# Kernel optimization log

Hardware: AMD Instinct MI355X
Metric: run time of the kernel (lower is better)

## Reference

```python
import jax, jax.numpy as jnp
import numpy as np

TOP_K = 2
NUM_EXPERTS = 64
AUX_COEF = 0.01


def setup_inputs() -> dict:
    key = jax.random.key(0)
    kx, kw = jax.random.split(key)
    B, S, D, E = 4, 4096, 2048, NUM_EXPERTS
    x = jax.random.normal(kx, (B, S, D), dtype=jnp.float32)
    # nn.Linear default init ~ U(-1/sqrt(D), 1/sqrt(D))
    W = jax.random.uniform(kw, (E, D), dtype=jnp.float32,
                           minval=-1.0 / np.sqrt(D), maxval=1.0 / np.sqrt(D))
    return {"x": x, "W": W}


def reference(x, W):
    B, S, D = x.shape
    E = W.shape[0]
    # router projection (no bias)
    logits = jnp.einsum('bsd,ed->bse', x, W)          # [B,S,E]
    probs = jax.nn.softmax(logits, axis=-1)           # [B,S,E]
    top_k_gates, top_k_indices = jax.lax.top_k(probs, TOP_K)  # [B,S,K]
    top_k_gates = top_k_gates / (jnp.sum(top_k_gates, axis=-1, keepdims=True) + 1e-9)
    # aux loss: fraction of routed slots per expert (one-hot mean) x mean router prob
    total_slots = B * S * TOP_K
    counts = jnp.zeros((E,), dtype=jnp.float32).at[top_k_indices.reshape(-1)].add(1.0)
    avg_tokens_per_expert = counts / total_slots      # == one_hot(idx).mean(dims 0,1,2)
    avg_router_prob = jnp.mean(probs, axis=(0, 1))    # [E]
    aux_loss = AUX_COEF * E * jnp.sum(avg_tokens_per_expert * avg_router_prob)
    return top_k_indices, top_k_gates, aux_loss
```

## Files before the change

### kernel.cpp

```cpp
#include <hip/hip_runtime.h>
#include <math.h>

#define NTOK 16384
#define DDIM 2048
#define NEXP 64
#define TM   16
#define NBLK (NTOK / TM)
#define NCH  32
#define NS   64

typedef _Float16 half4v __attribute__((ext_vector_type(4)));
typedef _Float16 half8v __attribute__((ext_vector_type(8)));
typedef float    f32x4  __attribute__((ext_vector_type(4)));

#define MFMA16(a, b, c) __builtin_amdgcn_mfma_f32_16x16x32_f16((a), (b), (c), 0, 0, 0)

__global__ __launch_bounds__(256) void prep_kernel(const float* __restrict__ W,
                                                   _Float16* __restrict__ Wh,
                                                   _Float16* __restrict__ Wl,
                                                   float* __restrict__ accg) {
    int idx = blockIdx.x * 256 + threadIdx.x;
    int e  = idx >> 8;
    int k0 = (idx & 255) << 3;
    const float* wp = W + (size_t)e * DDIM + k0;
    float4 w0 = *(const float4*)wp;
    float4 w1 = *(const float4*)(wp + 4);
    half8v h, l;
    h[0] = (_Float16)w0.x; l[0] = (_Float16)(w0.x - (float)h[0]);
    h[1] = (_Float16)w0.y; l[1] = (_Float16)(w0.y - (float)h[1]);
    h[2] = (_Float16)w0.z; l[2] = (_Float16)(w0.z - (float)h[2]);
    h[3] = (_Float16)w0.w; l[3] = (_Float16)(w0.w - (float)h[3]);
    h[4] = (_Float16)w1.x; l[4] = (_Float16)(w1.x - (float)h[4]);
    h[5] = (_Float16)w1.y; l[5] = (_Float16)(w1.y - (float)h[5]);
    h[6] = (_Float16)w1.z; l[6] = (_Float16)(w1.z - (float)h[6]);
    h[7] = (_Float16)w1.w; l[7] = (_Float16)(w1.w - (float)h[7]);
    int S = k0 >> 5, nb = e >> 4, nl = e & 15, q = (k0 >> 3) & 3;
    size_t off = (size_t)S * 2048 + nb * 512 + q * 128 + nl * 8;
    *(half8v*)&Wh[off] = h;
    *(half8v*)&Wl[off] = l;
    if (idx < 128) accg[idx] = 0.0f;
}

__device__ inline void cvt_store(_Float16* __restrict__ Hp, _Float16* __restrict__ Lp,
                                 int off, float4 v) {
    half4v h, l;
    h.x = (_Float16)v.x; l.x = (_Float16)(v.x - (float)h.x);
    h.y = (_Float16)v.y; l.y = (_Float16)(v.y - (float)h.y);
    h.z = (_Float16)v.z; l.z = (_Float16)(v.z - (float)h.z);
    h.w = (_Float16)v.w; l.w = (_Float16)(v.w - (float)h.w);
    *(half4v*)&Hp[off] = h;
    *(half4v*)&Lp[off] = l;
}

__global__ __launch_bounds__(256, 4) void router_kernel(
    const float* __restrict__ x, const _Float16* __restrict__ Wh,
    const _Float16* __restrict__ Wl, float* __restrict__ accg,
    float* __restrict__ out)
{
    __shared__ __align__(16) _Float16 Ah[2][1024];
    __shared__ __align__(16) _Float16 Al[2][1024];
    __shared__ float lgt[TM][NEXP + 1];
    __shared__ float cnt[NEXP];

    const int tid  = threadIdx.x;
    const int lane = tid & 63;
    const int wv   = __builtin_amdgcn_readfirstlane(tid >> 6);
    const int m0   = blockIdx.x * TM;

    if (tid < NEXP) cnt[tid] = 0.0f;

    const int tok0 = tid >> 4;
    const int kk0  = (tid & 15) * 4;
    const int s0   = kk0 >> 5, q0 = (kk0 >> 3) & 3, j00 = kk0 & 7;
    const int gW   = s0 * 64 + q0 * 16 + tok0;
    const int offA = ((gW ^ ((gW >> 4) & 7)) << 3) + j00;

    const int gr0 = lane;
    const int gr1 = 64 + lane;
    const int rdoff0 = (gr0 ^ ((gr0 >> 4) & 7)) << 3;
    const int rdoff1 = (gr1 ^ ((gr1 >> 4) & 7)) << 3;

    const float* gx = x + (size_t)(m0 + tok0) * DDIM + kk0;

    const _Float16* whp = Wh + wv * 512 + lane * 8;
    const _Float16* wlp = Wl + wv * 512 + lane * 8;

    f32x4 acc = {0.f, 0.f, 0.f, 0.f};

    float4 stg0 = *(const float4*)(gx);
    float4 stg1 = *(const float4*)(gx + 64);
    float4 stg2 = *(const float4*)(gx + 128);
    float4 stg3 = *(const float4*)(gx + 192);
    half8v wh0 = *(const half8v*)(whp);
    half8v wh1 = *(const half8v*)(whp + 2048);
    half8v wh2 = *(const half8v*)(whp + 4096);
    half8v wh3 = *(const half8v*)(whp + 6144);
    half8v wl0 = *(const half8v*)(wlp);
    half8v wl1 = *(const half8v*)(wlp + 2048);
    half8v wl2 = *(const half8v*)(wlp + 4096);
    half8v wl3 = *(const half8v*)(wlp + 6144);

#define CHUNK(ch, STG, P, WHA, WLA, WHB, WLB)                               \
    {                                                                        \
        cvt_store(&Ah[P][0], &Al[P][0], offA, STG);                          \
        const int cf = ((ch) + 4 < NCH) ? (ch) + 4 : 0;                      \
        STG = *(const float4*)(gx + cf * 64);                                \
        asm volatile("s_waitcnt lgkmcnt(0)" ::: "memory");                   \
        __builtin_amdgcn_s_barrier();                                        \
        {                                                \
            half8v ah = *(const half8v*)&Ah[P][rdoff0];                      \
            half8v al = *(const half8v*)&Al[P][rdoff0];                      \
            half8v bh = WHA, bl = WLA;                                       \
            const int SgN = (2 * (ch) + 4) & (NS - 1);                       \
            WHA = *(const half8v*)(whp + (size_t)SgN * 2048);                \
            WLA = *(const half8v*)(wlp + (size_t)SgN * 2048);                \
            acc = MFMA16(al, bh, acc);                                       \
            acc = MFMA16(ah, bl, acc);                                       \
            acc = MFMA16(ah, bh, acc);                                       \
        }                                                                    \
        {                                              \
            half8v ah = *(const half8v*)&Ah[P][rdoff1];                      \
            half8v al = *(const half8v*)&Al[P][rdoff1];                      \
            half8v bh = WHB, bl = WLB;                                       \
            const int SgN = (2 * (ch) + 5) & (NS - 1);                       \
            WHB = *(const half8v*)(whp + (size_t)SgN * 2048);                \
            WLB = *(const half8v*)(wlp + (size_t)SgN * 2048);                \
            acc = MFMA16(al, bh, acc);                                       \
            acc = MFMA16(ah, bl, acc);                                       \
            acc = MFMA16(ah, bh, acc);                                       \
        }                                                                    \
    }

    for (int cb = 0; cb < NCH; cb += 4) {
        CHUNK(cb + 0, stg0, 0, wh0, wl0, wh1, wl1);
        CHUNK(cb + 1, stg1, 1, wh2, wl2, wh3, wl3);
        CHUNK(cb + 2, stg2, 0, wh0, wl0, wh1, wl1);
        CHUNK(cb + 3, stg3, 1, wh2, wl2, wh3, wl3);
    }
#undef CHUNK

    {
        const int q  = lane >> 4;
        const int nl = lane & 15;
        #pragma unroll
        for (int r = 0; r < 4; ++r)
            lgt[q * 4 + r][wv * 16 + nl] = acc[r];
    }
    __syncthreads();

    if (tid < 128) {
        const int m = tid >> 3;
        const int j = tid & 7;
        float l[8];
        #pragma unroll
        for (int i = 0; i < 8; ++i) l[i] = lgt[m][j * 8 + i];

        float mx = l[0];
        #pragma unroll
        for (int i = 1; i < 8; ++i) mx = fmaxf(mx, l[i]);
        #pragma unroll
        for (int off = 1; off < 8; off <<= 1) mx = fmaxf(mx, __shfl_xor(mx, off, 8));

        float ev[8];
        float zs = 0.f;
        float v1 = -INFINITY, v2 = -INFINITY;
        int i1 = 0, i2 = 0;
        #pragma unroll
        for (int i = 0; i < 8; ++i) {
            ev[i] = __expf(l[i] - mx);
            zs += ev[i];
            int e = j * 8 + i;
            if (l[i] > v1)      { v2 = v1; i2 = i1; v1 = l[i]; i1 = e; }
            else if (l[i] > v2) { v2 = l[i]; i2 = e; }
        }
        #pragma unroll
        for (int off = 1; off < 8; off <<= 1) zs += __shfl_xor(zs, off, 8);

        #pragma unroll
        for (int off = 1; off < 8; off <<= 1) {
            float ov1 = __shfl_xor(v1, off, 8);
            int   oi1 = __shfl_xor(i1, off, 8);
            float ov2 = __shfl_xor(v2, off, 8);
            int   oi2 = __shfl_xor(i2, off, 8);
            bool afirst = (v1 > ov1) || (v1 == ov1 && i1 < oi1);
            if (afirst) {
                bool t = (v2 > ov1) || (v2 == ov1 && i2 < oi1);
                v2 = t ? v2 : ov1;
                i2 = t ? i2 : oi1;
            } else {
                bool t = (ov2 > v1) || (ov2 == v1 && oi2 < i1);
                v2 = t ? ov2 : v1;
                i2 = t ? oi2 : i1;
                v1 = ov1;
                i1 = oi1;
            }
        }

        const float invz = 1.0f / zs;
        if (j == 0) {
            float p1 = invz;
            float p2 = __expf(v2 - mx) * invz;
            float sden = p1 + p2 + 1e-9f;
            int tok = m0 + m;
            out[tok * 2 + 0] = (float)i1;
            out[tok * 2 + 1] = (float)i2;
            out[32768 + tok * 2 + 0] = p1 / sden;
            out[32768 + tok * 2 + 1] = p2 / sden;
            atomicAdd(&cnt[i1], 1.0f);
            atomicAdd(&cnt[i2], 1.0f);
        }

        #pragma unroll
        for (int i = 0; i < 8; ++i) lgt[m][j * 8 + i] = ev[i] * invz;
    }
    __syncthreads();

    if (tid < NEXP) {
        atomicAdd(&accg[tid], cnt[tid]);
    } else if (tid < 128) {
        int e = tid - 64;
        float s = 0.f;
        #pragma unroll
        for (int t = 0; t < TM; ++t) s += lgt[t][e];
        atomicAdd(&accg[64 + e], s);
    }
}

__global__ void finalize_kernel(const float* __restrict__ accg,
                                float* __restrict__ out)
{
    int t = threadIdx.x;
    float c = accg[t];
    float p = accg[64 + t];
    float term = (c / (float)(NTOK * 2)) * (p / (float)NTOK);
    #pragma unroll
    for (int off = 1; off < 64; off <<= 1) term += __shfl_xor(term, off, 64);
    if (t == 0) out[65536] = 0.01f * (float)NEXP * term;
}

extern "C" void kernel_launch(void* const* d_in, const int* in_sizes, int n_in,
                              void* d_out, int out_size, void* d_ws, size_t ws_size,
                              hipStream_t stream) {
    const float* x = (const float*)d_in[0];
    const float* W = (const float*)d_in[1];
    float* out  = (float*)d_out;
    float* accg = (float*)d_ws;
    _Float16* Wh = (_Float16*)(accg + 128);
    _Float16* Wl = Wh + (size_t)DDIM * NEXP;

    prep_kernel<<<64, 256, 0, stream>>>(W, Wh, Wl, accg);
    router_kernel<<<NBLK, 256, 0, stream>>>(x, Wh, Wl, accg, out);
    finalize_kernel<<<1, 64, 0, stream>>>(accg, out);
}
```

Measured before the change: 212.5 us.

## Grow router token tile to 64 so each W fragment feeds four MFMA tiles

Each block now handles 64 tokens instead of 16, with four accumulator tiles per wave, so every W hi/lo fragment loaded from global memory is reused across four token tiles instead of one. This cuts W reload traffic per token by 4x and lowers per-block overhead. The x staging now uses wider per-thread loads with prefetch distance 2, and a second barrier per chunk guards LDS buffer reuse. In exchange there are 4x fewer blocks (256), more LDS and registers per block, and launch bounds drop to one block per SM, which reduces occupancy and latency hiding.

```diff
diff --git a/kernel.cpp b/kernel.cpp
--- a/kernel.cpp
+++ b/kernel.cpp
@@ -4,12 +4,11 @@
 #define NTOK 16384
 #define DDIM 2048
 #define NEXP 64
-#define TM   16
-#define NBLK (NTOK / TM)
+#define TMB  64
+#define NBLK (NTOK / TMB)
 #define NCH  32
 #define NS   64
 
-typedef _Float16 half4v __attribute__((ext_vector_type(4)));
 typedef _Float16 half8v __attribute__((ext_vector_type(8)));
 typedef float    f32x4  __attribute__((ext_vector_type(4)));
 
@@ -41,56 +40,59 @@
     if (idx < 128) accg[idx] = 0.0f;
 }
 
-__device__ inline void cvt_store(_Float16* __restrict__ Hp, _Float16* __restrict__ Lp,
-                                 int off, float4 v) {
-    half4v h, l;
-    h.x = (_Float16)v.x; l.x = (_Float16)(v.x - (float)h.x);
-    h.y = (_Float16)v.y; l.y = (_Float16)(v.y - (float)h.y);
-    h.z = (_Float16)v.z; l.z = (_Float16)(v.z - (float)h.z);
-    h.w = (_Float16)v.w; l.w = (_Float16)(v.w - (float)h.w);
-    *(half4v*)&Hp[off] = h;
-    *(half4v*)&Lp[off] = l;
-}
-
-__global__ __launch_bounds__(256, 4) void router_kernel(
+__device__ __forceinline__ void cvt8(float4 a, float4 b, half8v& h, half8v& l) {
+    h[0]=(_Float16)a.x; l[0]=(_Float16)(a.x-(float)h[0]);
+    h[1]=(_Float16)a.y; l[1]=(_Float16)(a.y-(float)h[1]);
+    h[2]=(_Float16)a.z; l[2]=(_Float16)(a.z-(float)h[2]);
+    h[3]=(_Float16)a.w; l[3]=(_Float16)(a.w-(float)h[3]);
+    h[4]=(_Float16)b.x; l[4]=(_Float16)(b.x-(float)h[4]);
+    h[5]=(_Float16)b.y; l[5]=(_Float16)(b.y-(float)h[5]);
+    h[6]=(_Float16)b.z; l[6]=(_Float16)(b.z-(float)h[6]);
+    h[7]=(_Float16)b.w; l[7]=(_Float16)(b.w-(float)h[7]);
+}
+
+__global__ __launch_bounds__(256, 1) void router_kernel(
     const float* __restrict__ x, const _Float16* __restrict__ Wh,
     const _Float16* __restrict__ Wl, float* __restrict__ accg,
     float* __restrict__ out)
 {
-    __shared__ __align__(16) _Float16 Ah[2][1024];
-    __shared__ __align__(16) _Float16 Al[2][1024];
-    __shared__ float lgt[TM][NEXP + 1];
+    __shared__ __align__(16) _Float16 Ah[2][4096];
+    __shared__ __align__(16) _Float16 Al[2][4096];
+    __shared__ float lgt[TMB][NEXP + 1];
     __shared__ float cnt[NEXP];
 
     const int tid  = threadIdx.x;
     const int lane = tid & 63;
     const int wv   = __builtin_amdgcn_readfirstlane(tid >> 6);
-    const int m0   = blockIdx.x * TM;
+    const int m0   = blockIdx.x * TMB;
 
     if (tid < NEXP) cnt[tid] = 0.0f;
 
-    const int tok0 = tid >> 4;
-    const int kk0  = (tid & 15) * 4;
-    const int s0   = kk0 >> 5, q0 = (kk0 >> 3) & 3, j00 = kk0 & 7;
-    const int gW   = s0 * 64 + q0 * 16 + tok0;
-    const int offA = ((gW ^ ((gW >> 4) & 7)) << 3) + j00;
-
-    const int gr0 = lane;
+    const int r    = tid >> 2;
+    const int c0   = (tid & 3) * 16;
+    const int tile = r >> 4, tok = r & 15;
+    const int S0 = c0 >> 5,       q0 = (c0 >> 3) & 3;
+    const int S1 = (c0+8) >> 5,   q1 = ((c0+8) >> 3) & 3;
+    const int g0 = S0*64 + q0*16 + tok,  g1 = S1*64 + q1*16 + tok;
+    const int off0 = tile*1024 + (g0 ^ ((g0>>4)&7)) * 8;
+    const int off1 = tile*1024 + (g1 ^ ((g1>>4)&7)) * 8;
+
+    const float* gx = x + (size_t)(m0 + r) * DDIM + c0;
+
     const int gr1 = 64 + lane;
-    const int rdoff0 = (gr0 ^ ((gr0 >> 4) & 7)) << 3;
-    const int rdoff1 = (gr1 ^ ((gr1 >> 4) & 7)) << 3;
-
-    const float* gx = x + (size_t)(m0 + tok0) * DDIM + kk0;
+    const int rd0 = (lane ^ ((lane>>4)&7)) * 8;
+    const int rd1 = (gr1 ^ ((gr1>>4)&7)) * 8;
 
     const _Float16* whp = Wh + wv * 512 + lane * 8;
     const _Float16* wlp = Wl + wv * 512 + lane * 8;
 
-    f32x4 acc = {0.f, 0.f, 0.f, 0.f};
-
-    float4 stg0 = *(const float4*)(gx);
-    float4 stg1 = *(const float4*)(gx + 64);
-    float4 stg2 = *(const float4*)(gx + 128);
-    float4 stg3 = *(const float4*)(gx + 192);
+    f32x4 acc0 = {0.f,0.f,0.f,0.f}, acc1 = {0.f,0.f,0.f,0.f};
+    f32x4 acc2 = {0.f,0.f,0.f,0.f}, acc3 = {0.f,0.f,0.f,0.f};
+
+    float4 xa0 = *(const float4*)(gx +  0), xa1 = *(const float4*)(gx +  4);
+    float4 xa2 = *(const float4*)(gx +  8), xa3 = *(const float4*)(gx + 12);
+    float4 xb0 = *(const float4*)(gx + 64), xb1 = *(const float4*)(gx + 68);
+    float4 xb2 = *(const float4*)(gx + 72), xb3 = *(const float4*)(gx + 76);
     half8v wh0 = *(const half8v*)(whp);
     half8v wh1 = *(const half8v*)(whp + 2048);
     half8v wh2 = *(const half8v*)(whp + 4096);
@@ -100,56 +102,99 @@
     half8v wl2 = *(const half8v*)(wlp + 4096);
     half8v wl3 = *(const half8v*)(wlp + 6144);
 
-#define CHUNK(ch, STG, P, WHA, WLA, WHB, WLB)                               \
+#define CHUNK(ch, X0, X1, X2, X3, P, WHA, WLA, WHB, WLB)                    \
     {                                                                        \
-        cvt_store(&Ah[P][0], &Al[P][0], offA, STG);                          \
-        const int cf = ((ch) + 4 < NCH) ? (ch) + 4 : 0;                      \
-        STG = *(const float4*)(gx + cf * 64);                                \
+        half8v h_, l_;                                                       \
+        cvt8(X0, X1, h_, l_);                                                \
+        *(half8v*)&Ah[P][off0] = h_;  *(half8v*)&Al[P][off0] = l_;           \
+        cvt8(X2, X3, h_, l_);                                                \
+        *(half8v*)&Ah[P][off1] = h_;  *(half8v*)&Al[P][off1] = l_;           \
+        const int cf = ((ch) + 2 < NCH) ? (ch) + 2 : 0;                      \
+        X0 = *(const float4*)(gx + cf * 64 +  0);                            \
+        X1 = *(const float4*)(gx + cf * 64 +  4);                            \
+        X2 = *(const float4*)(gx + cf * 64 +  8);                            \
+        X3 = *(const float4*)(gx + cf * 64 + 12);                            \
         asm volatile("s_waitcnt lgkmcnt(0)" ::: "memory");                   \
         __builtin_amdgcn_s_barrier();                                        \
         {                                                \
-            half8v ah = *(const half8v*)&Ah[P][rdoff0];                      \
-            half8v al = *(const half8v*)&Al[P][rdoff0];                      \
+            half8v a0h = *(const half8v*)&Ah[P][   0 + rd0];                 \
+            half8v a0l = *(const half8v*)&Al[P][   0 + rd0];                 \
+            half8v a1h = *(const half8v*)&Ah[P][1024 + rd0];                 \
+            half8v a1l = *(const half8v*)&Al[P][1024 + rd0];                 \
+            half8v a2h = *(const half8v*)&Ah[P][2048 + rd0];                 \
+            half8v a2l = *(const half8v*)&Al[P][2048 + rd0];                 \
+            half8v a3h = *(const half8v*)&Ah[P][3072 + rd0];                 \
+            half8v a3l = *(const half8v*)&Al[P][3072 + rd0];                 \
             half8v bh = WHA, bl = WLA;                                       \
             const int SgN = (2 * (ch) + 4) & (NS - 1);                       \
             WHA = *(const half8v*)(whp + (size_t)SgN * 2048);                \
             WLA = *(const half8v*)(wlp + (size_t)SgN * 2048);                \
-            acc = MFMA16(al, bh, acc);                                       \
-            acc = MFMA16(ah, bl, acc);                                       \
-            acc = MFMA16(ah, bh, acc);                                       \
+            acc0 = MFMA16(a0l, bh, acc0);                                    \
+            acc0 = MFMA16(a0h, bl, acc0);                                    \
+            acc0 = MFMA16(a0h, bh, acc0);                                    \
+            acc1 = MFMA16(a1l, bh, acc1);                                    \
+            acc1 = MFMA16(a1h, bl, acc1);                                    \
+            acc1 = MFMA16(a1h, bh, acc1);                                    \
+            acc2 = MFMA16(a2l, bh, acc2);                                    \
+            acc2 = MFMA16(a2h, bl, acc2);                                    \
+            acc2 = MFMA16(a2h, bh, acc2);                                    \
+            acc3 = MFMA16(a3l, bh, acc3);                                    \
+            acc3 = MFMA16(a3h, bl, acc3);                                    \
+            acc3 = MFMA16(a3h, bh, acc3);                                    \
         }                                                                    \
         {                                              \
-            half8v ah = *(const half8v*)&Ah[P][rdoff1];                      \
-            half8v al = *(const half8v*)&Al[P][rdoff1];                      \
+            half8v a0h = *(const half8v*)&Ah[P][   0 + rd1];                 \
+            half8v a0l = *(const half8v*)&Al[P][   0 + rd1];                 \
+            half8v a1h = *(const half8v*)&Ah[P][1024 + rd1];                 \
+            half8v a1l = *(const half8v*)&Al[P][1024 + rd1];                 \
+            half8v a2h = *(const half8v*)&Ah[P][2048 + rd1];                 \
+            half8v a2l = *(const half8v*)&Al[P][2048 + rd1];                 \
+            half8v a3h = *(const half8v*)&Ah[P][3072 + rd1];                 \
+            half8v a3l = *(const half8v*)&Al[P][3072 + rd1];                 \
             half8v bh = WHB, bl = WLB;                                       \
             const int SgN = (2 * (ch) + 5) & (NS - 1);                       \
             WHB = *(const half8v*)(whp + (size_t)SgN * 2048);                \
             WLB = *(const half8v*)(wlp + (size_t)SgN * 2048);                \
-            acc = MFMA16(al, bh, acc);                                       \
-            acc = MFMA16(ah, bl, acc);                                       \
-            acc = MFMA16(ah, bh, acc);                                       \
+            acc0 = MFMA16(a0l, bh, acc0);                                    \
+            acc0 = MFMA16(a0h, bl, acc0);                                    \
+            acc0 = MFMA16(a0h, bh, acc0);                                    \
+            acc1 = MFMA16(a1l, bh, acc1);                                    \
+            acc1 = MFMA16(a1h, bl, acc1);                                    \
+            acc1 = MFMA16(a1h, bh, acc1);                                    \
+            acc2 = MFMA16(a2l, bh, acc2);                                    \
+            acc2 = MFMA16(a2h, bl, acc2);                                    \
+            acc2 = MFMA16(a2h, bh, acc2);                                    \
+            acc3 = MFMA16(a3l, bh, acc3);                                    \
+            acc3 = MFMA16(a3h, bl, acc3);                                    \
+            acc3 = MFMA16(a3h, bh, acc3);                                    \
         }                                                                    \
-    }
-
-    for (int cb = 0; cb < NCH; cb += 4) {
-        CHUNK(cb + 0, stg0, 0, wh0, wl0, wh1, wl1);
-        CHUNK(cb + 1, stg1, 1, wh2, wl2, wh3, wl3);
-        CHUNK(cb + 2, stg2, 0, wh0, wl0, wh1, wl1);
-        CHUNK(cb + 3, stg3, 1, wh2, wl2, wh3, wl3);
+        \
+        asm volatile("s_waitcnt lgkmcnt(0)" ::: "memory");                   \
+        __builtin_amdgcn_s_barrier();                                        \
+    }
+
+    for (int cb = 0; cb < NCH; cb += 2) {
+        CHUNK(cb + 0, xa0, xa1, xa2, xa3, 0, wh0, wl0, wh1, wl1);
+        CHUNK(cb + 1, xb0, xb1, xb2, xb3, 1, wh2, wl2, wh3, wl3);
     }
 #undef CHUNK
 
     {
-        const int q  = lane >> 4;
+        const int qr = lane >> 4;
         const int nl = lane & 15;
         #pragma unroll
-        for (int r = 0; r < 4; ++r)
-            lgt[q * 4 + r][wv * 16 + nl] = acc[r];
+        for (int rr = 0; rr < 4; ++rr) {
+            const int mm = qr * 4 + rr;
+            lgt[ 0 + mm][wv * 16 + nl] = acc0[rr];
+            lgt[16 + mm][wv * 16 + nl] = acc1[rr];
+            lgt[32 + mm][wv * 16 + nl] = acc2[rr];
+            lgt[48 + mm][wv * 16 + nl] = acc3[rr];
+        }
     }
     __syncthreads();
 
-    if (tid < 128) {
-        const int m = tid >> 3;
+    for (int pass = 0; pass < 2; ++pass) {
+        const int m = pass * 32 + (tid >> 3);
         const int j = tid & 7;
         float l[8];
         #pragma unroll
@@ -201,11 +246,11 @@
             float p1 = invz;
             float p2 = __expf(v2 - mx) * invz;
             float sden = p1 + p2 + 1e-9f;
-            int tok = m0 + m;
-            out[tok * 2 + 0] = (float)i1;
-            out[tok * 2 + 1] = (float)i2;
-            out[32768 + tok * 2 + 0] = p1 / sden;
-            out[32768 + tok * 2 + 1] = p2 / sden;
+            int tokg = m0 + m;
+            out[tokg * 2 + 0] = (float)i1;
+            out[tokg * 2 + 1] = (float)i2;
+            out[32768 + tokg * 2 + 0] = p1 / sden;
+            out[32768 + tokg * 2 + 1] = p2 / sden;
             atomicAdd(&cnt[i1], 1.0f);
             atomicAdd(&cnt[i2], 1.0f);
         }
@@ -221,7 +266,7 @@
         int e = tid - 64;
         float s = 0.f;
         #pragma unroll
-        for (int t = 0; t < TM; ++t) s += lgt[t][e];
+        for (int t = 0; t < TMB; ++t) s += lgt[t][e];
         atomicAdd(&accg[64 + e], s);
     }
 }
```

New measurement: 207.2 us (median of 2 runs). -2.5%, faster.
